# Kernel optimization log

Measured on AMD Instinct MI355X. Metric: run time of the kernel, lower is better.

## Reference

```python
import jax, jax.numpy as jnp
import numpy as np

HIDDEN = 1024
RANK = 4
N_TASKS = 5
LORA_SCALING = 1.0 / RANK  # lora_alpha / lora_rank = 1/4
LN_EPS = 1e-5


def setup_inputs() -> dict:
    key = jax.random.key(0)
    ks = jax.random.split(key, 9)
    B, S, D = 16, 2048, HIDDEN
    hidden_states = jax.random.normal(ks[0], (B, S, D), dtype=jnp.float32)
    input_tensor = jax.random.normal(ks[1], (B, S, D), dtype=jnp.float32)
    adapter_mask = jax.random.randint(ks[2], (B,), 0, N_TASKS, dtype=jnp.int32)
    W = jax.random.normal(ks[3], (D, D), dtype=jnp.float32) * 0.02
    b = jax.random.normal(ks[4], (D,), dtype=jnp.float32) * 0.02
    lora_A = jax.random.normal(ks[5], (N_TASKS, RANK, D), dtype=jnp.float32) * 0.02
    lora_B = jax.random.normal(ks[6], (N_TASKS, D, RANK), dtype=jnp.float32) * 0.02
    gamma = jnp.ones((D,), dtype=jnp.float32)
    beta = jnp.zeros((D,), dtype=jnp.float32)
    return {
        "hidden_states": hidden_states,
        "input_tensor": input_tensor,
        "W": W,
        "b": b,
        "lora_A": lora_A,
        "lora_B": lora_B,
        "gamma": gamma,
        "beta": beta,
        "adapter_mask": adapter_mask,
    }


def _layernorm(x, gamma, beta):
    mu = jnp.mean(x, axis=-1, keepdims=True)
    xc = x - mu
    var = jnp.mean(xc * xc, axis=-1, keepdims=True)
    return xc * jax.lax.rsqrt(var + LN_EPS) * gamma + beta


def reference(hidden_states, input_tensor, W, b, lora_A, lora_B, gamma, beta, adapter_mask):
    # Base dense projection (first self.dense call)
    h1 = jnp.einsum("bsd,ed->bse", hidden_states, W) + b  # [B,S,D]
    # Per-task LoRA-parametrized dense applied to the projected states
    # (the source loops over unique tasks with gather/scatter; vectorized here
    #  by gathering each batch row's adapter).
    base2 = jnp.einsum("bsd,ed->bse", h1, W) + b  # [B,S,D]
    A_b = lora_A[adapter_mask]  # [B, r, D]
    B_b = lora_B[adapter_mask]  # [B, D, r]
    low = jnp.einsum("bsd,brd->bsr", h1, A_b)  # [B,S,r]
    delta = jnp.einsum("bsr,bdr->bsd", low, B_b)  # [B,S,D]
    h2 = base2 + LORA_SCALING * delta
    # dropout is identity in eval / p=0; residual + LayerNorm
    return _layernorm(h2 + input_tensor, gamma, beta)
```

## Files before the change

### kernel.cpp

```cpp
#include <hip/hip_runtime.h>
#include <hip/hip_bf16.h>
#include <stdint.h>

#define D_HID 1024
#define M_TOT 32768
#define LN_EPS 1e-5f

typedef __bf16 bf16x8 __attribute__((ext_vector_type(8)));
typedef float f32x4 __attribute__((ext_vector_type(4)));
typedef unsigned short u16;
typedef u16 u16x8 __attribute__((ext_vector_type(8)));
typedef u16 u16x4v __attribute__((ext_vector_type(4)));

__device__ __forceinline__ float bf2f(u16 x) {
  union { unsigned int u; float f; } c; c.u = ((unsigned int)x) << 16; return c.f;
}
__device__ __forceinline__ u16 f2bf(float f) {
  union { __bf16 h; u16 u; } c; c.h = (__bf16)f; return c.u;
}
__device__ __forceinline__ u16x8 cvt8(const float* g) {
  float4 f0 = *(const float4*)g;
  float4 f1 = *(const float4*)(g + 4);
  u16x8 v;
  v[0] = f2bf(f0.x); v[1] = f2bf(f0.y); v[2] = f2bf(f0.z); v[3] = f2bf(f0.w);
  v[4] = f2bf(f1.x); v[5] = f2bf(f1.y); v[6] = f2bf(f1.z); v[7] = f2bf(f1.w);
  return v;
}
__device__ __forceinline__ void gld16(const u16* g, u16* lds_wave_base) {
  __builtin_amdgcn_global_load_lds(
      (__attribute__((address_space(1))) unsigned int*)g,
      (__attribute__((address_space(3))) unsigned int*)lds_wave_base, 16, 0, 0);
}

__global__ __launch_bounds__(256) void s1_prep(
    const float* __restrict__ hs, u16* __restrict__ hs_bf,
    const float* __restrict__ W, u16* __restrict__ hi, u16* __restrict__ lo,
    u16* __restrict__ hiT, u16* __restrict__ loT,
    const float* __restrict__ lA, u16* __restrict__ lAh, u16* __restrict__ lAl) {
  __shared__ float tile[32][33];
  const int bid = blockIdx.x, tid = threadIdx.x;
  if (bid < 2048) {
    int i = bid * 256 + tid;
#pragma unroll
    for (int it = 0; it < 8; ++it, i += 2048 * 256)
      *(u16x8*)(hs_bf + (size_t)i * 8) = cvt8(hs + (size_t)i * 8);
    return;
  }
  if (bid >= 3072) {
    const int b = bid - 3072;
    for (int i = tid; i < 16 * 1024; i += 256) {
      const int r = b * 16 + (i >> 10), c = i & 1023;
      const float v = (r < 20) ? lA[(size_t)r * 1024 + c] : 0.f;
      const u16 h = f2bf(v);
      lAh[(size_t)r * 1024 + c] = h;
      lAl[(size_t)r * 1024 + c] = f2bf(v - bf2f(h));
    }
    return;
  }
  const int rb = bid - 2048;
  const int bj = rb & 31, bi = rb >> 5;
  const int tx = tid & 31, ty = tid >> 5;
#pragma unroll
  for (int r0 = 0; r0 < 32; r0 += 8) {
    const int r = r0 + ty;
    const size_t o = (size_t)(bi * 32 + r) * D_HID + bj * 32 + tx;
    const float v = W[o];
    tile[r][tx] = v;
    const u16 h = f2bf(v);
    hi[o] = h; lo[o] = f2bf(v - bf2f(h));
  }
  __syncthreads();
#pragma unroll
  for (int r0 = 0; r0 < 32; r0 += 8) {
    const int r = r0 + ty;
    const float v = tile[tx][r];
    const size_t o = (size_t)(bj * 32 + r) * D_HID + bi * 32 + tx;
    const u16 h = f2bf(v);
    hiT[o] = h; loT[o] = f2bf(v - bf2f(h));
  }
}

__global__ __launch_bounds__(256, 1) void s2_gemm(
    const u16* __restrict__ Ah, const u16* __restrict__ Al,
    const u16* __restrict__ Bh, const u16* __restrict__ Bl,
    const u16* __restrict__ lAh, const u16* __restrict__ lAl,
    float* __restrict__ C, float* __restrict__ A2) {
  __shared__ __align__(16) u16 sAh[128 * 32], sAl[128 * 32];
  __shared__ __align__(16) u16 sBh[128 * 32], sBl[128 * 32];
  const int bid = blockIdx.x, tid = threadIdx.x, wave = tid >> 6, lane = tid & 63;
  const int by = bid >> 3, bx = bid & 7;
  const bool isA2 = (by == 8);
  const u16* Asrc_h = isA2 ? lAh : Ah;
  const u16* Asrc_l = isA2 ? lAl : Al;
  const int rowbase = isA2 ? 0 : by * 128;
  const int srow = tid >> 2, scol = (tid & 3) * 8;
  size_t aOff = (size_t)(rowbase + srow) * D_HID + scol;
  size_t bOff = (size_t)(bx * 128 + srow) * D_HID + scol;
  const int wb = wave * 512;
  const int wm = wave >> 1, wn = wave & 1;
  const int mrow = lane & 15, quad = lane >> 4;
  const int fA = (wm * 64 + mrow) * 32 + quad * 8;
  const int fB = (wn * 64 + mrow) * 32 + quad * 8;
  f32x4 acc[4][4];
#pragma unroll
  for (int i = 0; i < 4; ++i)
#pragma unroll
    for (int j = 0; j < 4; ++j) acc[i][j] = (f32x4){0.f, 0.f, 0.f, 0.f};
  for (int k0 = 0; k0 < D_HID; k0 += 32) {
    __syncthreads();
    gld16(Asrc_h + aOff, sAh + wb); gld16(Asrc_h + aOff + 64 * D_HID, sAh + wb + 2048);
    gld16(Asrc_l + aOff, sAl + wb); gld16(Asrc_l + aOff + 64 * D_HID, sAl + wb + 2048);
    gld16(Bh + bOff, sBh + wb); gld16(Bh + bOff + 64 * D_HID, sBh + wb + 2048);
    gld16(Bl + bOff, sBl + wb); gld16(Bl + bOff + 64 * D_HID, sBl + wb + 2048);
    aOff += 32; bOff += 32;
    __syncthreads();
    bf16x8 ah[4], al4[4], bh[4], bl4[4];
#pragma unroll
    for (int m = 0; m < 4; ++m) {
      ah[m]  = *(const bf16x8*)(sAh + fA + m * 512);
      al4[m] = *(const bf16x8*)(sAl + fA + m * 512);
    }
#pragma unroll
    for (int n = 0; n < 4; ++n) {
      bh[n]  = *(const bf16x8*)(sBh + fB + n * 512);
      bl4[n] = *(const bf16x8*)(sBl + fB + n * 512);
    }
#pragma unroll
    for (int m = 0; m < 4; ++m)
#pragma unroll
      for (int n = 0; n < 4; ++n) {
        acc[m][n] = __builtin_amdgcn_mfma_f32_16x16x32_bf16(ah[m],  bh[n],  acc[m][n], 0, 0, 0);
        acc[m][n] = __builtin_amdgcn_mfma_f32_16x16x32_bf16(al4[m], bh[n],  acc[m][n], 0, 0, 0);
        acc[m][n] = __builtin_amdgcn_mfma_f32_16x16x32_bf16(ah[m],  bl4[n], acc[m][n], 0, 0, 0);
      }
  }
  const int nBase = bx * 128 + wn * 64;
#pragma unroll
  for (int m = 0; m < 4; ++m)
#pragma unroll
    for (int n = 0; n < 4; ++n) {
      const int nn = nBase + n * 16 + mrow;
#pragma unroll
      for (int r = 0; r < 4; ++r) {
        const int lr = wm * 64 + m * 16 + quad * 4 + r;
        if (!isA2) {
          C[(size_t)(by * 128 + lr) * D_HID + nn] = acc[m][n][r];
        } else if (lr < 20) {
          A2[(size_t)lr * D_HID + nn] = acc[m][n][r];
        }
      }
    }
}

__global__ __launch_bounds__(256) void weff_beff(
    const float* __restrict__ Wc, const float* __restrict__ A2,
    const float* __restrict__ lB, const float* __restrict__ lA,
    const float* __restrict__ W, const float* __restrict__ bvec,
    u16* __restrict__ Weff, float* __restrict__ beff) {
  const int n = blockIdx.x, t = blockIdx.y, tid = threadIdx.x;
  const int wave = tid >> 6, lane = tid & 63;
  float br[4];
#pragma unroll
  for (int r = 0; r < 4; ++r) br[r] = lB[(size_t)t * 4096 + n * 4 + r];
  float4 v = *(const float4*)(Wc + (size_t)n * D_HID + tid * 4);
#pragma unroll
  for (int r = 0; r < 4; ++r) {
    const float4 a2 = *(const float4*)(A2 + (size_t)(t * 4 + r) * D_HID + tid * 4);
    const float s = 0.25f * br[r];
    v.x += s * a2.x; v.y += s * a2.y; v.z += s * a2.z; v.w += s * a2.w;
  }
  u16x4v o; o[0] = f2bf(v.x); o[1] = f2bf(v.y); o[2] = f2bf(v.z); o[3] = f2bf(v.w);
  *(u16x4v*)(Weff + (size_t)t * 1048576 + (size_t)n * D_HID + tid * 4) = o;
  const float4 bb = *(const float4*)(bvec + tid * 4);
  float p[5];
  {
    const float4 wr = *(const float4*)(W + (size_t)n * D_HID + tid * 4);
    p[0] = wr.x * bb.x + wr.y * bb.y + wr.z * bb.z + wr.w * bb.w;
  }
#pragma unroll
  for (int r = 0; r < 4; ++r) {
    const float4 ar = *(const float4*)(lA + (size_t)(t * 4 + r) * D_HID + tid * 4);
    p[1 + r] = ar.x * bb.x + ar.y * bb.y + ar.z * bb.z + ar.w * bb.w;
  }
#pragma unroll
  for (int m = 1; m < 64; m <<= 1)
#pragma unroll
    for (int j = 0; j < 5; ++j) p[j] += __shfl_xor(p[j], m);
  __shared__ float red[4][5];
  if (lane == 0)
#pragma unroll
    for (int j = 0; j < 5; ++j) red[wave][j] = p[j];
  __syncthreads();
  if (tid == 0) {
    float P = 0.f, Cr[4] = {0.f, 0.f, 0.f, 0.f};
#pragma unroll
    for (int w = 0; w < 4; ++w) {
      P += red[w][0];
#pragma unroll
      for (int r = 0; r < 4; ++r) Cr[r] += red[w][1 + r];
    }
    float e = 0.f;
#pragma unroll
    for (int r = 0; r < 4; ++r) e += br[r] * Cr[r];
    beff[t * D_HID + n] = P + bvec[n] + 0.25f * e;
  }
}

template <int VM>
__device__ __forceinline__ void kstep(const u16* sAc, const u16* sBc,
                                      int fA, int fB, f32x4 (&acc)[4][4]) {
  asm volatile("s_waitcnt vmcnt(%0)" :: "n"(VM) : "memory");
  __builtin_amdgcn_s_barrier();
  __builtin_amdgcn_sched_barrier(0);
  bf16x8 af[4], bfr[4];
#pragma unroll
  for (int m = 0; m < 4; ++m) af[m]  = *(const bf16x8*)(sAc + fA + m * 512);
#pragma unroll
  for (int n = 0; n < 4; ++n) bfr[n] = *(const bf16x8*)(sBc + fB + n * 512);
  asm volatile("s_waitcnt lgkmcnt(0)" ::: "memory");
  __builtin_amdgcn_sched_barrier(0);
  __builtin_amdgcn_s_barrier();
  __builtin_amdgcn_sched_barrier(0);
  __builtin_amdgcn_s_setprio(1);
#pragma unroll
  for (int m = 0; m < 4; ++m)
#pragma unroll
    for (int n = 0; n < 4; ++n)
      acc[m][n] = __builtin_amdgcn_mfma_f32_16x16x32_bf16(af[m], bfr[n], acc[m][n], 0, 0, 0);
  __builtin_amdgcn_s_setprio(0);
}

__global__ __launch_bounds__(256, 3) void gemm_main(
    const u16* __restrict__ A, const u16* __restrict__ Wf,
    const float* __restrict__ beff, const float* __restrict__ resid,
    const int* __restrict__ mask, float* __restrict__ out) {
  __shared__ __align__(16) u16 sA[3][4096], sB[3][4096];
  const int tid = threadIdx.x, wave = tid >> 6, lane = tid & 63;
  const int L = blockIdx.x;
  const int by = (L & 7) * 32 + (L >> 6);
  const int bx = (L >> 3) & 7;
  const int task = mask[by >> 4];
  const u16* Bt = Wf + (size_t)task * (D_HID * D_HID);
  const int srow = tid >> 2, scol = (tid & 3) * 8;
  size_t aOff = (size_t)(by * 128 + srow) * D_HID + scol;
  size_t bOff = (size_t)(bx * 128 + srow) * D_HID + scol;
  const int wb = wave * 512;
  const int wm = wave >> 1, wn = wave & 1;
  const int mrow = lane & 15, quad = lane >> 4;
  const int fA = (wm * 64 + mrow) * 32 + quad * 8;
  const int fB = (wn * 64 + mrow) * 32 + quad * 8;
  f32x4 acc[4][4];
#pragma unroll
  for (int i = 0; i < 4; ++i)
#pragma unroll
    for (int j = 0; j < 4; ++j) acc[i][j] = (f32x4){0.f, 0.f, 0.f, 0.f};

  auto stage = [&](int buf) {
    gld16(A + aOff,               &sA[buf][wb]);
    gld16(A + aOff + 64 * D_HID,  &sA[buf][wb + 2048]);
    gld16(Bt + bOff,              &sB[buf][wb]);
    gld16(Bt + bOff + 64 * D_HID, &sB[buf][wb + 2048]);
    aOff += 32; bOff += 32;
  };

  stage(0);
  stage(1);
  int cur = 0;
  for (int t = 0; t < 30; ++t) {
    int sb = cur + 2; if (sb >= 3) sb -= 3;
    stage(sb);
    kstep<8>(&sA[cur][0], &sB[cur][0], fA, fB, acc);
    if (++cur == 3) cur = 0;
  }
  kstep<4>(&sA[cur][0], &sB[cur][0], fA, fB, acc);
  if (++cur == 3) cur = 0;
  kstep<0>(&sA[cur][0], &sB[cur][0], fA, fB, acc);

  const float* bb = beff + task * D_HID;
  const size_t mBase = (size_t)by * 128 + wm * 64;
  const int nBase = bx * 128 + wn * 64;
#pragma unroll
  for (int mf = 0; mf < 4; ++mf)
#pragma unroll
    for (int nf = 0; nf < 4; ++nf) {
      const int n = nBase + nf * 16 + mrow;
      const float bval = bb[n];
#pragma unroll
      for (int r = 0; r < 4; ++r) {
        const size_t m = mBase + mf * 16 + quad * 4 + r;
        out[m * D_HID + n] = acc[mf][nf][r] + bval + resid[m * D_HID + n];
      }
    }
}

__global__ __launch_bounds__(256) void ln4(float* __restrict__ io,
                                           const float* __restrict__ gamma,
                                           const float* __restrict__ beta) {
  const int row = blockIdx.x * 4 + (threadIdx.x >> 6);
  const int lane = threadIdx.x & 63;
  float* p = io + (size_t)row * D_HID + lane * 16;
  float4 v0 = ((const float4*)p)[0], v1 = ((const float4*)p)[1];
  float4 v2 = ((const float4*)p)[2], v3 = ((const float4*)p)[3];
  float s = v0.x + v0.y + v0.z + v0.w + v1.x + v1.y + v1.z + v1.w
          + v2.x + v2.y + v2.z + v2.w + v3.x + v3.y + v3.z + v3.w;
  float q = v0.x*v0.x + v0.y*v0.y + v0.z*v0.z + v0.w*v0.w
          + v1.x*v1.x + v1.y*v1.y + v1.z*v1.z + v1.w*v1.w
          + v2.x*v2.x + v2.y*v2.y + v2.z*v2.z + v2.w*v2.w
          + v3.x*v3.x + v3.y*v3.y + v3.z*v3.z + v3.w*v3.w;
#pragma unroll
  for (int m = 1; m < 64; m <<= 1) { s += __shfl_xor(s, m); q += __shfl_xor(q, m); }
  const float mu  = s * (1.f / (float)D_HID);
  const float var = q * (1.f / (float)D_HID) - mu * mu;
  const float inv = rsqrtf(var + LN_EPS);
  const float4* gp = (const float4*)(gamma + lane * 16);
  const float4* bp = (const float4*)(beta + lane * 16);
  float4 g, bbv, o;
#define LNW(k, vk) \
  g = gp[k]; bbv = bp[k]; \
  o.x = (vk.x - mu) * inv * g.x + bbv.x; o.y = (vk.y - mu) * inv * g.y + bbv.y; \
  o.z = (vk.z - mu) * inv * g.z + bbv.z; o.w = (vk.w - mu) * inv * g.w + bbv.w; \
  ((float4*)p)[k] = o;
  LNW(0, v0) LNW(1, v1) LNW(2, v2) LNW(3, v3)
#undef LNW
}

extern "C" void kernel_launch(void* const* d_in, const int* in_sizes, int n_in,
                              void* d_out, int out_size, void* d_ws, size_t ws_size,
                              hipStream_t stream) {
  const float* hs    = (const float*)d_in[0];
  const float* inp   = (const float*)d_in[1];
  const float* W     = (const float*)d_in[2];
  const float* b     = (const float*)d_in[3];
  const float* lA    = (const float*)d_in[4];
  const float* lB    = (const float*)d_in[5];
  const float* gamma = (const float*)d_in[6];
  const float* beta  = (const float*)d_in[7];
  const int*   mask  = (const int*)d_in[8];
  float* out = (float*)d_out;

  char* wsb = (char*)d_ws;
  u16*   hs_bf = (u16*)wsb;
  float* Wc    = (float*)(wsb + 67108864);
  u16*   weff  = (u16*)(wsb + 71303168);
  u16*   Whi   = weff;
  u16*   Wlo   = weff + 1048576;
  u16*   WhiT  = weff + 2097152;
  u16*   WloT  = weff + 3145728;
  u16*   lAh   = weff + 4194304;
  u16*   lAl   = weff + 4325376;
  float* A2    = (float*)(wsb + 81788928);
  float* beff  = (float*)(wsb + 81871360);

  s1_prep<<<3080, 256, 0, stream>>>(hs, hs_bf, W, Whi, Wlo, WhiT, WloT, lA, lAh, lAl);
  s2_gemm<<<72, 256, 0, stream>>>(Whi, Wlo, WhiT, WloT, lAh, lAl, Wc, A2);
  weff_beff<<<dim3(1024, 5), 256, 0, stream>>>(Wc, A2, lB, lA, W, b, weff, beff);
  gemm_main<<<2048, 256, 0, stream>>>(hs_bf, weff, beff, inp, mask, out);
  ln4<<<M_TOT / 4, 256, 0, stream>>>(out, gamma, beta);
}
```

Before: 556.7 us.

## Rewrite main GEMM with 256x256 tiles, 8 waves, swizzled LDS and interleaved prefetch

The main bf16 GEMM moves from 128x128 tiles with 4 waves and a 3-stage K=32 ring to 256x256 tiles with 8 waves, K=64 double-buffered LDS using an XOR swizzle, and loads of the next tile split into quarters and interleaved between four MFMA phases. Larger tiles raise arithmetic intensity and cut global/L2 traffic per FLOP, and the swizzle is meant to avoid LDS bank conflicts. In exchange, occupancy drops to one 512-thread block per CU, only 512 blocks are launched, and register pressure rises with 128 accumulator floats per thread.

Result: no change. 548.3 us (-1.5%).

```diff
diff --git a/kernel.cpp b/kernel.cpp
--- a/kernel.cpp
+++ b/kernel.cpp
@@ -105,7 +105,7 @@
 #pragma unroll
   for (int i = 0; i < 4; ++i)
 #pragma unroll
-    for (int j = 0; j < 4; ++j) acc[i][j] = (f32x4){0.f, 0.f, 0.f, 0.f};
+    for (int jn = 0; jn < 4; ++jn) acc[i][jn] = (f32x4){0.f, 0.f, 0.f, 0.f};
   for (int k0 = 0; k0 < D_HID; k0 += 32) {
     __syncthreads();
     gld16(Asrc_h + aOff, sAh + wb); gld16(Asrc_h + aOff + 64 * D_HID, sAh + wb + 2048);
@@ -185,11 +185,11 @@
 #pragma unroll
   for (int m = 1; m < 64; m <<= 1)
 #pragma unroll
-    for (int j = 0; j < 5; ++j) p[j] += __shfl_xor(p[j], m);
+    for (int jj = 0; jj < 5; ++jj) p[jj] += __shfl_xor(p[jj], m);
   __shared__ float red[4][5];
   if (lane == 0)
 #pragma unroll
-    for (int j = 0; j < 5; ++j) red[wave][j] = p[j];
+    for (int jj = 0; jj < 5; ++jj) red[wave][jj] = p[jj];
   __syncthreads();
   if (tid == 0) {
     float P = 0.f, Cr[4] = {0.f, 0.f, 0.f, 0.f};
@@ -199,91 +199,174 @@
 #pragma unroll
       for (int r = 0; r < 4; ++r) Cr[r] += red[w][1 + r];
     }
-    float e = 0.f;
-#pragma unroll
-    for (int r = 0; r < 4; ++r) e += br[r] * Cr[r];
+    const float e = br[0]*Cr[0] + br[1]*Cr[1] + br[2]*Cr[2] + br[3]*Cr[3];
     beff[t * D_HID + n] = P + bvec[n] + 0.25f * e;
   }
 }
 
-template <int VM>
-__device__ __forceinline__ void kstep(const u16* sAc, const u16* sBc,
-                                      int fA, int fB, f32x4 (&acc)[4][4]) {
-  asm volatile("s_waitcnt vmcnt(%0)" :: "n"(VM) : "memory");
+__global__ __launch_bounds__(512, 1) void gemm_main(
+    const u16* __restrict__ Ag, const u16* __restrict__ Wf,
+    const float* __restrict__ beff, const float* __restrict__ resid,
+    const int* __restrict__ mask, float* __restrict__ out) {
+  __shared__ __align__(16) u16 sAf[2 * 16384];
+  __shared__ __align__(16) u16 sBf[2 * 16384];
+  const int tid = threadIdx.x, wave = tid >> 6, lane = tid & 63;
+  const int L = blockIdx.x;
+  const int xcd = L & 7, j = L >> 3;
+  const int bx = j & 3;
+  const int by = xcd * 16 + (j >> 2);
+  const int task = mask[by >> 3];
+  const u16* Bg = Wf + (size_t)task * (D_HID * D_HID);
+
+  const int acol = ((lane & 7) ^ (lane >> 3)) * 8;
+  const int aBase = (by * 256 + wave * 8 + (lane >> 3)) * D_HID + acol;
+  const int bBase = (bx * 256 + wave * 8 + (lane >> 3)) * D_HID + acol;
+
+  auto stageA = [&](int ktar, int half) {
+#pragma unroll
+    for (int q = 0; q < 2; ++q)
+      gld16(Ag + (aBase + ktar * 64 + half * 131072 + q * 65536),
+            sAf + ((ktar & 1) * 16384 + half * 8192 + q * 4096 + wave * 512));
+  };
+  auto stageB = [&](int ktar, int half) {
+#pragma unroll
+    for (int q = 0; q < 2; ++q)
+      gld16(Bg + (bBase + ktar * 64 + half * 131072 + q * 65536),
+            sBf + ((ktar & 1) * 16384 + half * 8192 + q * 4096 + wave * 512));
+  };
+
+  const int wm = wave >> 2, wn = wave & 3;
+  const int l15 = lane & 15, quad = lane >> 4, l7 = lane & 7;
+  const int vA0 = (wm * 128 + l15) * 64 + ((quad ^ l7) * 8);
+  const int vB0 = (wn * 64 + l15) * 64 + ((quad ^ l7) * 8);
+
+  f32x4 acc[8][4];
+#pragma unroll
+  for (int i = 0; i < 8; ++i)
+#pragma unroll
+    for (int jn = 0; jn < 4; ++jn) acc[i][jn] = (f32x4){0.f, 0.f, 0.f, 0.f};
+
+  stageB(0, 0); stageB(0, 1); stageA(0, 0); stageA(0, 1);
+  stageB(1, 0); stageA(1, 0);
+  asm volatile("s_waitcnt vmcnt(4)" ::: "memory");
   __builtin_amdgcn_s_barrier();
   __builtin_amdgcn_sched_barrier(0);
-  bf16x8 af[4], bfr[4];
-#pragma unroll
-  for (int m = 0; m < 4; ++m) af[m]  = *(const bf16x8*)(sAc + fA + m * 512);
-#pragma unroll
-  for (int n = 0; n < 4; ++n) bfr[n] = *(const bf16x8*)(sBc + fB + n * 512);
-  asm volatile("s_waitcnt lgkmcnt(0)" ::: "memory");
-  __builtin_amdgcn_sched_barrier(0);
-  __builtin_amdgcn_s_barrier();
-  __builtin_amdgcn_sched_barrier(0);
-  __builtin_amdgcn_s_setprio(1);
-#pragma unroll
-  for (int m = 0; m < 4; ++m)
-#pragma unroll
-    for (int n = 0; n < 4; ++n)
-      acc[m][n] = __builtin_amdgcn_mfma_f32_16x16x32_bf16(af[m], bfr[n], acc[m][n], 0, 0, 0);
-  __builtin_amdgcn_s_setprio(0);
-}
-
-__global__ __launch_bounds__(256, 3) void gemm_main(
-    const u16* __restrict__ A, const u16* __restrict__ Wf,
-    const float* __restrict__ beff, const float* __restrict__ resid,
-    const int* __restrict__ mask, float* __restrict__ out) {
-  __shared__ __align__(16) u16 sA[3][4096], sB[3][4096];
-  const int tid = threadIdx.x, wave = tid >> 6, lane = tid & 63;
-  const int L = blockIdx.x;
-  const int by = (L & 7) * 32 + (L >> 6);
-  const int bx = (L >> 3) & 7;
-  const int task = mask[by >> 4];
-  const u16* Bt = Wf + (size_t)task * (D_HID * D_HID);
-  const int srow = tid >> 2, scol = (tid & 3) * 8;
-  size_t aOff = (size_t)(by * 128 + srow) * D_HID + scol;
-  size_t bOff = (size_t)(bx * 128 + srow) * D_HID + scol;
-  const int wb = wave * 512;
-  const int wm = wave >> 1, wn = wave & 1;
-  const int mrow = lane & 15, quad = lane >> 4;
-  const int fA = (wm * 64 + mrow) * 32 + quad * 8;
-  const int fB = (wn * 64 + mrow) * 32 + quad * 8;
-  f32x4 acc[4][4];
-#pragma unroll
-  for (int i = 0; i < 4; ++i)
-#pragma unroll
-    for (int j = 0; j < 4; ++j) acc[i][j] = (f32x4){0.f, 0.f, 0.f, 0.f};
-
-  auto stage = [&](int buf) {
-    gld16(A + aOff,               &sA[buf][wb]);
-    gld16(A + aOff + 64 * D_HID,  &sA[buf][wb + 2048]);
-    gld16(Bt + bOff,              &sB[buf][wb]);
-    gld16(Bt + bOff + 64 * D_HID, &sB[buf][wb + 2048]);
-    aOff += 32; bOff += 32;
-  };
-
-  stage(0);
-  stage(1);
-  int cur = 0;
-  for (int t = 0; t < 30; ++t) {
-    int sb = cur + 2; if (sb >= 3) sb -= 3;
-    stage(sb);
-    kstep<8>(&sA[cur][0], &sB[cur][0], fA, fB, acc);
-    if (++cur == 3) cur = 0;
-  }
-  kstep<4>(&sA[cur][0], &sB[cur][0], fA, fB, acc);
-  if (++cur == 3) cur = 0;
-  kstep<0>(&sA[cur][0], &sB[cur][0], fA, fB, acc);
+
+  bf16x8 a[4][2], b[4][2];
+#pragma unroll 1
+  for (int k2 = 0; k2 < 8; ++k2) {
+#pragma unroll
+    for (int par = 0; par < 2; ++par) {
+      const int kt = k2 * 2 + par;
+      const u16* pA = sAf + par * 16384;
+      const u16* pB = sBf + par * 16384;
+      const bool st01 = (par == 0) || (k2 < 7);
+      const bool st23 = (k2 < 7);
+
+#pragma unroll
+      for (int m4 = 0; m4 < 4; ++m4) {
+        a[m4][0] = *(const bf16x8*)(pA + (vA0 + m4 * 1024));
+        a[m4][1] = *(const bf16x8*)(pA + ((vA0 ^ 32) + m4 * 1024));
+      }
+#pragma unroll
+      for (int n2 = 0; n2 < 2; ++n2) {
+        b[n2][0] = *(const bf16x8*)(pB + (vB0 + n2 * 1024));
+        b[n2][1] = *(const bf16x8*)(pB + ((vB0 ^ 32) + n2 * 1024));
+      }
+      if (st01) stageB(kt + 1, 1);
+      __builtin_amdgcn_s_barrier();
+      asm volatile("s_waitcnt lgkmcnt(0)" ::: "memory");
+      __builtin_amdgcn_sched_barrier(0);
+      __builtin_amdgcn_s_setprio(1);
+#pragma unroll
+      for (int m4 = 0; m4 < 4; ++m4)
+#pragma unroll
+        for (int n2 = 0; n2 < 2; ++n2)
+#pragma unroll
+          for (int kk = 0; kk < 2; ++kk)
+            acc[m4][n2] = __builtin_amdgcn_mfma_f32_16x16x32_bf16(
+                a[m4][kk], b[n2][kk], acc[m4][n2], 0, 0, 0);
+      __builtin_amdgcn_s_setprio(0);
+      __builtin_amdgcn_s_barrier();
+      __builtin_amdgcn_sched_barrier(0);
+
+#pragma unroll
+      for (int n2 = 0; n2 < 2; ++n2) {
+        b[2 + n2][0] = *(const bf16x8*)(pB + (vB0 + (2 + n2) * 1024));
+        b[2 + n2][1] = *(const bf16x8*)(pB + ((vB0 ^ 32) + (2 + n2) * 1024));
+      }
+      if (st01) stageA(kt + 1, 1);
+      __builtin_amdgcn_s_barrier();
+      asm volatile("s_waitcnt lgkmcnt(0)" ::: "memory");
+      __builtin_amdgcn_sched_barrier(0);
+      __builtin_amdgcn_s_setprio(1);
+#pragma unroll
+      for (int m4 = 0; m4 < 4; ++m4)
+#pragma unroll
+        for (int n2 = 0; n2 < 2; ++n2)
+#pragma unroll
+          for (int kk = 0; kk < 2; ++kk)
+            acc[m4][2 + n2] = __builtin_amdgcn_mfma_f32_16x16x32_bf16(
+                a[m4][kk], b[2 + n2][kk], acc[m4][2 + n2], 0, 0, 0);
+      __builtin_amdgcn_s_setprio(0);
+      __builtin_amdgcn_s_barrier();
+      __builtin_amdgcn_sched_barrier(0);
+
+#pragma unroll
+      for (int m4 = 0; m4 < 4; ++m4) {
+        a[m4][0] = *(const bf16x8*)(pA + (vA0 + (4 + m4) * 1024));
+        a[m4][1] = *(const bf16x8*)(pA + ((vA0 ^ 32) + (4 + m4) * 1024));
+      }
+      if (st23) stageB(kt + 2, 0);
+      __builtin_amdgcn_s_barrier();
+      asm volatile("s_waitcnt lgkmcnt(0)" ::: "memory");
+      __builtin_amdgcn_sched_barrier(0);
+      __builtin_amdgcn_s_setprio(1);
+#pragma unroll
+      for (int m4 = 0; m4 < 4; ++m4)
+#pragma unroll
+        for (int n2 = 0; n2 < 2; ++n2)
+#pragma unroll
+          for (int kk = 0; kk < 2; ++kk)
+            acc[4 + m4][n2] = __builtin_amdgcn_mfma_f32_16x16x32_bf16(
+                a[m4][kk], b[n2][kk], acc[4 + m4][n2], 0, 0, 0);
+      __builtin_amdgcn_s_setprio(0);
+      __builtin_amdgcn_s_barrier();
+      __builtin_amdgcn_sched_barrier(0);
+
+      if (st23) stageA(kt + 2, 0);
+      if (par == 0) {
+        if (k2 < 7) { asm volatile("s_waitcnt vmcnt(4)" ::: "memory"); }
+        else        { asm volatile("s_waitcnt vmcnt(0)" ::: "memory"); }
+      } else {
+        if (k2 < 7) { asm volatile("s_waitcnt vmcnt(4)" ::: "memory"); }
+      }
+      __builtin_amdgcn_s_barrier();
+      asm volatile("s_waitcnt lgkmcnt(0)" ::: "memory");
+      __builtin_amdgcn_sched_barrier(0);
+      __builtin_amdgcn_s_setprio(1);
+#pragma unroll
+      for (int m4 = 0; m4 < 4; ++m4)
+#pragma unroll
+        for (int n2 = 0; n2 < 2; ++n2)
+#pragma unroll
+          for (int kk = 0; kk < 2; ++kk)
+            acc[4 + m4][2 + n2] = __builtin_amdgcn_mfma_f32_16x16x32_bf16(
+                a[m4][kk], b[2 + n2][kk], acc[4 + m4][2 + n2], 0, 0, 0);
+      __builtin_amdgcn_s_setprio(0);
+      __builtin_amdgcn_s_barrier();
+      __builtin_amdgcn_sched_barrier(0);
+    }
+  }
 
   const float* bb = beff + task * D_HID;
-  const size_t mBase = (size_t)by * 128 + wm * 64;
-  const int nBase = bx * 128 + wn * 64;
-#pragma unroll
-  for (int mf = 0; mf < 4; ++mf)
+  const size_t mBase = (size_t)by * 256 + wm * 128;
+  const int nb0 = bx * 256 + wn * 64;
+#pragma unroll
+  for (int mf = 0; mf < 8; ++mf)
 #pragma unroll
     for (int nf = 0; nf < 4; ++nf) {
-      const int n = nBase + nf * 16 + mrow;
+      const int n = nb0 + nf * 16 + l15;
       const float bval = bb[n];
 #pragma unroll
       for (int r = 0; r < 4; ++r) {
@@ -354,6 +437,6 @@
   s1_prep<<<3080, 256, 0, stream>>>(hs, hs_bf, W, Whi, Wlo, WhiT, WloT, lA, lAh, lAl);
   s2_gemm<<<72, 256, 0, stream>>>(Whi, Wlo, WhiT, WloT, lAh, lAl, Wc, A2);
   weff_beff<<<dim3(1024, 5), 256, 0, stream>>>(Wc, A2, lB, lA, W, b, weff, beff);
-  gemm_main<<<2048, 256, 0, stream>>>(hs_bf, weff, beff, inp, mask, out);
+  gemm_main<<<512, 512, 0, stream>>>(hs_bf, weff, beff, inp, mask, out);
   ln4<<<M_TOT / 4, 256, 0, stream>>>(out, gamma, beta);
 }
```
